# Kernel optimization log

Hardware: AMD Instinct MI355X
Metric: run time of the kernel (lower is better)

The kernel has to match this reference:

```python
import jax, jax.numpy as jnp
import numpy as np

NHLOG2PI = -0.5 * np.log(2.0 * np.pi)


def _log_bessel_i(nu, x):
    # log I_nu(x) via the uniform asymptotic expansion (A&S 9.7.7), accurate for large nu.
    # Replaces the original mpmath besseli loop with a device-friendly closed form.
    z = x / nu
    sq = jnp.sqrt(1.0 + z * z)
    eta = sq + jnp.log(z) - jnp.log1p(sq)
    t = 1.0 / sq
    u1 = (3.0 * t - 5.0 * t ** 3) / 24.0  # first correction term
    return nu * eta - 0.5 * jnp.log(2.0 * jnp.pi * nu) - 0.25 * jnp.log1p(z * z) + jnp.log1p(u1 / nu)


def _log_vmf_partition(d, kappa):
    # log C_d(kappa) = d*(-0.5 log 2pi) + s*log(kappa) - log I_s(kappa), s = d/2 - 1
    s = 0.5 * d - 1.0
    return d * NHLOG2PI + s * jnp.log(kappa) - _log_bessel_i(s, kappa)


def reference(id_samples, kappa_weight, prototypes, targets, project_dim):
    eps_n = 1e-12  # torch F.normalize eps
    eps_c = 1e-8   # torch cosine_similarity eps
    # --- sequential normalized EMA scatter-update of prototypes (faithful to per-sample loop) ---
    norm_samples = id_samples / jnp.maximum(
        jnp.linalg.norm(id_samples, axis=-1, keepdims=True), eps_n)

    def step(protos, inp):
        s_n, t = inp
        new = 0.05 * s_n + 0.95 * protos[t]
        new = new / jnp.maximum(jnp.linalg.norm(new), eps_n)
        return protos.at[t].set(new), None

    protos, _ = jax.lax.scan(step, prototypes, (norm_samples, targets))
    protos = jax.lax.stop_gradient(protos)  # original uses .data.detach()

    # --- cosine similarity [N, C] without materializing the repeated tensors ---
    x_n = id_samples / jnp.maximum(jnp.linalg.norm(id_samples, axis=-1, keepdims=True), eps_c)
    p_n = protos / jnp.maximum(jnp.linalg.norm(protos, axis=-1, keepdims=True), eps_c)
    cos = x_n @ p_n.T  # [N, C]

    kap = jax.nn.relu(kappa_weight)  # [C]
    logits = cos * kap[None, :]
    weight_before_exp = jnp.exp(_log_vmf_partition(float(project_dim), kap))[None, :]  # [1, C]

    # --- weighted vMF NLL ---
    num = weight_before_exp * jnp.exp(logits)
    pred = num / num.sum(-1, keepdims=True)
    p_t = jnp.take_along_axis(pred, targets[:, None], axis=1)[:, 0]
    return -jnp.mean(jnp.log(p_t + 1e-6))


def setup_inputs() -> dict:
    key = jax.random.key(0)
    k1, k2, k3 = jax.random.split(key, 3)
    N, C, D = 16384, 2048, 32
    return {
        "id_samples": jax.random.normal(k1, (N, D), dtype=jnp.float32),
        "kappa_weight": jax.random.uniform(k2, (C,), dtype=jnp.float32),
        "prototypes": jnp.zeros((C, D), dtype=jnp.float32),
        "targets": jax.random.randint(k3, (N,), 0, C),
        "project_dim": D,
    }
```

## Files before the change

### kernel.cpp

```cpp
#include <hip/hip_runtime.h>
#include <hip/hip_bf16.h>
#include <math.h>

#define D 32
#define CAP 64
#define PRE 24
#define PBW 8
#define SBT 512
#define SSM 16

typedef __attribute__((ext_vector_type(8))) short short8v;
typedef __attribute__((ext_vector_type(4))) float float4v;

static __device__ __forceinline__ unsigned short f2bf(float f) {
    union { __hip_bfloat16 h; unsigned short u; } cv;
    cv.h = __float2bfloat16(f);
    return cv.u;
}

__global__ void __launch_bounds__(64 * PBW)
k_pb(const float* __restrict__ x, const int* __restrict__ tgt,
     const float* __restrict__ p_in, const float* __restrict__ kw,
     unsigned short* __restrict__ qb, float* __restrict__ w,
     int N, int C, float dval) {
    __shared__ int lcnt[PBW];
    __shared__ int llist[PBW][CAP];
    int tid = threadIdx.x, b = blockIdx.x;
    int lane = tid & 63, wv = tid >> 6;
    int c0 = b * PBW;

    if (tid < PBW) lcnt[tid] = 0;
    __syncthreads();
    for (int i = tid; i < N; i += 64 * PBW) {
        int t = tgt[i];
        int r = t - c0;
        if ((unsigned)r < (unsigned)PBW) {
            int pos = atomicAdd(&lcnt[r], 1);
            if (pos < CAP) llist[r][pos] = i;
        }
    }
    __syncthreads();

    int c = c0 + wv;
    int e = lane & 31;
    float p = p_in[(size_t)c * D + e];
    int count = lcnt[wv];

    if (count <= PRE) {
        int idx = (lane < count) ? llist[wv][lane] : 0x7fffffff;
        int rank = 0;
        for (int j = 0; j < count; ++j) {
            int v = __shfl(idx, j);
            rank += (v < idx) ? 1 : 0;
        }
        int sorted = 0;
        for (int j = 0; j < count; ++j) {
            int v = __shfl(idx, j); int r = __shfl(rank, j);
            if (r == lane) sorted = v;
        }
        float vals[PRE];
#pragma unroll
        for (int it = 0; it < PRE; ++it)
            if (it < count) {
                int si = __shfl(sorted, it);
                vals[it] = x[(size_t)si * D + e];
            }
#pragma unroll
        for (int it = 0; it < PRE; ++it)
            if (it < count) {
                float v = vals[it];
                float ss = v * v;
                ss += __shfl_xor(ss, 16); ss += __shfl_xor(ss, 8); ss += __shfl_xor(ss, 4);
                ss += __shfl_xor(ss, 2);  ss += __shfl_xor(ss, 1);
                vals[it] = v / fmaxf(sqrtf(ss), 1e-12f);
            }
#pragma unroll
        for (int it = 0; it < PRE; ++it)
            if (it < count) {
                p = fmaf(0.05f, vals[it], 0.95f * p);
                float pp = p * p;
                pp += __shfl_xor(pp, 16); pp += __shfl_xor(pp, 8); pp += __shfl_xor(pp, 4);
                pp += __shfl_xor(pp, 2);  pp += __shfl_xor(pp, 1);
                p = p / fmaxf(sqrtf(pp), 1e-12f);
            }
    } else if (count <= CAP) {
        int idx = (lane < count) ? llist[wv][lane] : 0x7fffffff;
        for (int it = 0; it < count; ++it) {
            int mn = idx;
            mn = min(mn, __shfl_xor(mn, 32)); mn = min(mn, __shfl_xor(mn, 16));
            mn = min(mn, __shfl_xor(mn, 8));  mn = min(mn, __shfl_xor(mn, 4));
            mn = min(mn, __shfl_xor(mn, 2));  mn = min(mn, __shfl_xor(mn, 1));
            float v = x[(size_t)mn * D + e];
            float ss = v * v;
            ss += __shfl_xor(ss, 16); ss += __shfl_xor(ss, 8); ss += __shfl_xor(ss, 4);
            ss += __shfl_xor(ss, 2);  ss += __shfl_xor(ss, 1);
            float s = v / fmaxf(sqrtf(ss), 1e-12f);
            p = fmaf(0.05f, s, 0.95f * p);
            float pp = p * p;
            pp += __shfl_xor(pp, 16); pp += __shfl_xor(pp, 8); pp += __shfl_xor(pp, 4);
            pp += __shfl_xor(pp, 2);  pp += __shfl_xor(pp, 1);
            p = p / fmaxf(sqrtf(pp), 1e-12f);
            if (idx == mn) idx = 0x7fffffff;
        }
    } else {
        for (int ii = 0; ii < N; ii += 64) {
            unsigned long long m = __ballot(tgt[ii + lane] == c);
            while (m) {
                int j = __ffsll(m) - 1;
                m &= (m - 1);
                float v = x[(size_t)(ii + j) * D + e];
                float ss = v * v;
                ss += __shfl_xor(ss, 16); ss += __shfl_xor(ss, 8); ss += __shfl_xor(ss, 4);
                ss += __shfl_xor(ss, 2);  ss += __shfl_xor(ss, 1);
                float s = v / fmaxf(sqrtf(ss), 1e-12f);
                p = fmaf(0.05f, s, 0.95f * p);
                float pp = p * p;
                pp += __shfl_xor(pp, 16); pp += __shfl_xor(pp, 8); pp += __shfl_xor(pp, 4);
                pp += __shfl_xor(pp, 2);  pp += __shfl_xor(pp, 1);
                p = p / fmaxf(sqrtf(pp), 1e-12f);
            }
        }
    }

    float pp = p * p;
    pp += __shfl_xor(pp, 16); pp += __shfl_xor(pp, 8); pp += __shfl_xor(pp, 4);
    pp += __shfl_xor(pp, 2);  pp += __shfl_xor(pp, 1);
    float pn = p / fmaxf(sqrtf(pp), 1e-8f);
    float kap = fmaxf(kw[c], 0.0f);
    if (lane < D) qb[(size_t)c * D + e] = f2bf(kap * pn);
    if (lane == 0) {
        float nu = 0.5f * dval - 1.0f;
        float z  = kap / nu, z2 = z * z;
        float sq = sqrtf(1.0f + z2);
        float t  = 1.0f / sq;
        float u1 = (3.0f * t - 5.0f * t * t * t) * (1.0f / 24.0f);
        float lw = dval * (-0.918938533204672742f)
                 + nu * (logf(nu) + log1pf(sq) - sq)
                 + 0.5f * logf(6.2831853071795864f * nu)
                 + 0.25f * log1pf(z2)
                 - log1pf(u1 / nu);
        w[c] = __expf(lw);
    }
}

__global__ void __launch_bounds__(SBT)
k_score(const float* __restrict__ x, const int* __restrict__ tgt,
        const unsigned short* __restrict__ qb, const float* __restrict__ w,
        float* __restrict__ part, int N, int C) {
    __shared__ float Sl[8][SSM];
    __shared__ float Lt[SSM];
    int tid = threadIdx.x, b = blockIdx.x;
    int lane = tid & 63, wv = tid >> 6;
    int m = lane & 15, kg = lane >> 4, k0 = kg * 8;
    int s0 = b * SSM;

    short8v a0;
    {
        const float4* px = (const float4*)(x + (size_t)(s0 + m) * D + k0);
        float4 u0 = px[0], u1 = px[1];
        float ss = u0.x*u0.x + u0.y*u0.y + u0.z*u0.z + u0.w*u0.w
                 + u1.x*u1.x + u1.y*u1.y + u1.z*u1.z + u1.w*u1.w;
        ss += __shfl_xor(ss, 16); ss += __shfl_xor(ss, 32);
        float inv = 1.0f / fmaxf(sqrtf(ss), 1e-8f);
        a0[0] = (short)f2bf(u0.x*inv); a0[1] = (short)f2bf(u0.y*inv);
        a0[2] = (short)f2bf(u0.z*inv); a0[3] = (short)f2bf(u0.w*inv);
        a0[4] = (short)f2bf(u1.x*inv); a0[5] = (short)f2bf(u1.y*inv);
        a0[6] = (short)f2bf(u1.z*inv); a0[7] = (short)f2bf(u1.w*inv);
    }

    int tr0[4];
#pragma unroll
    for (int r = 0; r < 4; ++r) tr0[r] = tgt[s0 + kg * 4 + r];

    float4v z = {0.f, 0.f, 0.f, 0.f};
    float4v sa0 = z;
    int ntiles = C >> 7;
    for (int jt = 0; jt < ntiles; ++jt) {
        int c0 = (wv * ntiles + jt) * 16;
        short8v bfrag = *(const short8v*)(qb + (size_t)(c0 + m) * D + k0);
        float wl = w[c0 + m];
        float4v acc0 = __builtin_amdgcn_mfma_f32_16x16x32_bf16(a0, bfrag, z, 0, 0, 0);
#pragma unroll
        for (int r = 0; r < 4; ++r) {
            if (c0 + m == tr0[r]) Lt[kg * 4 + r] = acc0[r];
            sa0[r] = fmaf(wl, __expf(acc0[r]), sa0[r]);
        }
    }
#pragma unroll
    for (int off = 1; off < 16; off <<= 1) {
#pragma unroll
        for (int r = 0; r < 4; ++r) sa0[r] += __shfl_xor(sa0[r], off);
    }
    if (m == 0) {
#pragma unroll
        for (int r = 0; r < 4; ++r) Sl[wv][kg * 4 + r] = sa0[r];
    }
    __syncthreads();

    if (wv == 0) {
        float val = 0.f;
        if (lane < SSM) {
            int s = lane;
            float S = ((Sl[0][s] + Sl[1][s]) + (Sl[2][s] + Sl[3][s]))
                    + ((Sl[4][s] + Sl[5][s]) + (Sl[6][s] + Sl[7][s]));
            int t = tgt[s0 + s];
            val = logf(w[t] * __expf(Lt[s]) / S + 1e-6f);
        }
        val += __shfl_xor(val, 32); val += __shfl_xor(val, 16); val += __shfl_xor(val, 8);
        val += __shfl_xor(val, 4);  val += __shfl_xor(val, 2);  val += __shfl_xor(val, 1);
        if (lane == 0) part[b] = val;
    }
}

__global__ void k_out(const float* __restrict__ part, float* __restrict__ out,
                      int N, int nblk) {
    __shared__ float red[8];
    int tid = threadIdx.x, lane = tid & 63, wv = tid >> 6;
    float v = 0.f;
    if (tid < nblk)       v += part[tid];
    if (tid + 512 < nblk) v += part[tid + 512];
    v += __shfl_xor(v, 32); v += __shfl_xor(v, 16); v += __shfl_xor(v, 8);
    v += __shfl_xor(v, 4);  v += __shfl_xor(v, 2);  v += __shfl_xor(v, 1);
    if (lane == 0) red[wv] = v;
    __syncthreads();
    if (tid == 0)
        out[0] = -(((red[0] + red[1]) + (red[2] + red[3]))
                 + ((red[4] + red[5]) + (red[6] + red[7]))) / (float)N;
}

extern "C" void kernel_launch(void* const* d_in, const int* in_sizes, int n_in,
                              void* d_out, int out_size, void* d_ws, size_t ws_size,
                              hipStream_t stream) {
    const float* x    = (const float*)d_in[0];
    const float* kw   = (const float*)d_in[1];
    const float* p_in = (const float*)d_in[2];
    const int*   tgt  = (const int*)d_in[3];
    int C = in_sizes[1];
    int N = in_sizes[3];
    float dval = (float)(in_sizes[2] / C);
    int nblk = N / SSM;

    unsigned short* qb = (unsigned short*)d_ws;
    float* w    = (float*)(qb + (size_t)C * D);
    float* part = w + C;
    (void)n_in; (void)out_size; (void)ws_size;

    k_pb<<<C / PBW, 64 * PBW, 0, stream>>>(x, tgt, p_in, kw, qb, w, N, C, dval);
    k_score<<<nblk, SBT, 0, stream>>>(x, tgt, qb, w, part, N, C);
    k_out<<<1, 512, 0, stream>>>(part, (float*)d_out, N, nblk);
}
```

Before: 41.37 us.

## Map one thread per prototype class in EMA kernel with vectorized row loads

Restructures the prototype EMA kernel so each thread owns one class and keeps its 32-dim prototype in registers, instead of one 64-lane wavefront per class. Sample rows are read as float4 vectors, and per-class sample indices are ordered by a selection scan over shared memory. This removes the cross-lane shuffle reductions, the idle half-wave and most of the repeated full-target scanning, since far fewer blocks each scan the target list. In exchange the grid shrinks to a handful of blocks and each thread runs a serial chain of dependent-latency loads. A class with more than 33 samples falls back to a very slow serial scan over all targets.

Result: slower. 57.64 us (+39.3%).

```diff
diff --git a/kernel.cpp b/kernel.cpp
--- a/kernel.cpp
+++ b/kernel.cpp
@@ -3,9 +3,8 @@
 #include <math.h>
 
 #define D 32
-#define CAP 64
-#define PRE 24
-#define PBW 8
+#define CAP 33
+#define PBT 256
 #define SBT 512
 #define SSM 16
 
@@ -18,117 +17,105 @@
     return cv.u;
 }
 
-__global__ void __launch_bounds__(64 * PBW)
+static __device__ __forceinline__ void ema_step(float p[D], const float* __restrict__ x, int idx) {
+    float r0[D];
+#pragma unroll
+    for (int j = 0; j < D / 4; ++j) {
+        float4 v = ((const float4*)(x + (size_t)idx * D))[j];
+        r0[4*j] = v.x; r0[4*j+1] = v.y; r0[4*j+2] = v.z; r0[4*j+3] = v.w;
+    }
+    float s0 = 0.f, s1 = 0.f, s2 = 0.f, s3 = 0.f;
+#pragma unroll
+    for (int j = 0; j < D / 4; ++j) {
+        s0 = fmaf(r0[4*j],   r0[4*j],   s0);
+        s1 = fmaf(r0[4*j+1], r0[4*j+1], s1);
+        s2 = fmaf(r0[4*j+2], r0[4*j+2], s2);
+        s3 = fmaf(r0[4*j+3], r0[4*j+3], s3);
+    }
+    float inv = 1.0f / fmaxf(sqrtf((s0 + s1) + (s2 + s3)), 1e-12f);
+    float c05 = 0.05f * inv;
+#pragma unroll
+    for (int j = 0; j < D; ++j) p[j] = fmaf(c05, r0[j], 0.95f * p[j]);
+    float q0 = 0.f, q1 = 0.f, q2 = 0.f, q3 = 0.f;
+#pragma unroll
+    for (int j = 0; j < D / 4; ++j) {
+        q0 = fmaf(p[4*j],   p[4*j],   q0);
+        q1 = fmaf(p[4*j+1], p[4*j+1], q1);
+        q2 = fmaf(p[4*j+2], p[4*j+2], q2);
+        q3 = fmaf(p[4*j+3], p[4*j+3], q3);
+    }
+    float inv2 = 1.0f / fmaxf(sqrtf((q0 + q1) + (q2 + q3)), 1e-12f);
+#pragma unroll
+    for (int j = 0; j < D; ++j) p[j] *= inv2;
+}
+
+__global__ void __launch_bounds__(PBT)
 k_pb(const float* __restrict__ x, const int* __restrict__ tgt,
      const float* __restrict__ p_in, const float* __restrict__ kw,
      unsigned short* __restrict__ qb, float* __restrict__ w,
      int N, int C, float dval) {
-    __shared__ int lcnt[PBW];
-    __shared__ int llist[PBW][CAP];
+    __shared__ int lcnt[PBT];
+    __shared__ int llist[PBT][CAP];
     int tid = threadIdx.x, b = blockIdx.x;
-    int lane = tid & 63, wv = tid >> 6;
-    int c0 = b * PBW;
-
-    if (tid < PBW) lcnt[tid] = 0;
-    __syncthreads();
-    for (int i = tid; i < N; i += 64 * PBW) {
+    int c0 = b * PBT;
+    int c = c0 + tid;
+
+    lcnt[tid] = 0;
+    __syncthreads();
+#pragma unroll 4
+    for (int i = tid; i < N; i += PBT) {
         int t = tgt[i];
         int r = t - c0;
-        if ((unsigned)r < (unsigned)PBW) {
+        if ((unsigned)r < (unsigned)PBT) {
             int pos = atomicAdd(&lcnt[r], 1);
             if (pos < CAP) llist[r][pos] = i;
         }
     }
     __syncthreads();
 
-    int c = c0 + wv;
-    int e = lane & 31;
-    float p = p_in[(size_t)c * D + e];
-    int count = lcnt[wv];
-
-    if (count <= PRE) {
-        int idx = (lane < count) ? llist[wv][lane] : 0x7fffffff;
-        int rank = 0;
-        for (int j = 0; j < count; ++j) {
-            int v = __shfl(idx, j);
-            rank += (v < idx) ? 1 : 0;
-        }
-        int sorted = 0;
-        for (int j = 0; j < count; ++j) {
-            int v = __shfl(idx, j); int r = __shfl(rank, j);
-            if (r == lane) sorted = v;
-        }
-        float vals[PRE];
-#pragma unroll
-        for (int it = 0; it < PRE; ++it)
-            if (it < count) {
-                int si = __shfl(sorted, it);
-                vals[it] = x[(size_t)si * D + e];
+    int cnt = lcnt[tid];
+
+    float p[D];
+#pragma unroll
+    for (int j = 0; j < D / 4; ++j) {
+        float4 v = ((const float4*)(p_in + (size_t)c * D))[j];
+        p[4*j] = v.x; p[4*j+1] = v.y; p[4*j+2] = v.z; p[4*j+3] = v.w;
+    }
+
+    if (cnt <= CAP) {
+        int last = -1;
+        for (int step = 0; step < cnt; ++step) {
+            int best = 0x7fffffff;
+            for (int k = 0; k < cnt; ++k) {
+                int v = llist[tid][k];
+                if (v > last && v < best) best = v;
             }
-#pragma unroll
-        for (int it = 0; it < PRE; ++it)
-            if (it < count) {
-                float v = vals[it];
-                float ss = v * v;
-                ss += __shfl_xor(ss, 16); ss += __shfl_xor(ss, 8); ss += __shfl_xor(ss, 4);
-                ss += __shfl_xor(ss, 2);  ss += __shfl_xor(ss, 1);
-                vals[it] = v / fmaxf(sqrtf(ss), 1e-12f);
-            }
-#pragma unroll
-        for (int it = 0; it < PRE; ++it)
-            if (it < count) {
-                p = fmaf(0.05f, vals[it], 0.95f * p);
-                float pp = p * p;
-                pp += __shfl_xor(pp, 16); pp += __shfl_xor(pp, 8); pp += __shfl_xor(pp, 4);
-                pp += __shfl_xor(pp, 2);  pp += __shfl_xor(pp, 1);
-                p = p / fmaxf(sqrtf(pp), 1e-12f);
-            }
-    } else if (count <= CAP) {
-        int idx = (lane < count) ? llist[wv][lane] : 0x7fffffff;
-        for (int it = 0; it < count; ++it) {
-            int mn = idx;
-            mn = min(mn, __shfl_xor(mn, 32)); mn = min(mn, __shfl_xor(mn, 16));
-            mn = min(mn, __shfl_xor(mn, 8));  mn = min(mn, __shfl_xor(mn, 4));
-            mn = min(mn, __shfl_xor(mn, 2));  mn = min(mn, __shfl_xor(mn, 1));
-            float v = x[(size_t)mn * D + e];
-            float ss = v * v;
-            ss += __shfl_xor(ss, 16); ss += __shfl_xor(ss, 8); ss += __shfl_xor(ss, 4);
-            ss += __shfl_xor(ss, 2);  ss += __shfl_xor(ss, 1);
-            float s = v / fmaxf(sqrtf(ss), 1e-12f);
-            p = fmaf(0.05f, s, 0.95f * p);
-            float pp = p * p;
-            pp += __shfl_xor(pp, 16); pp += __shfl_xor(pp, 8); pp += __shfl_xor(pp, 4);
-            pp += __shfl_xor(pp, 2);  pp += __shfl_xor(pp, 1);
-            p = p / fmaxf(sqrtf(pp), 1e-12f);
-            if (idx == mn) idx = 0x7fffffff;
+            last = best;
+            ema_step(p, x, best);
         }
     } else {
-        for (int ii = 0; ii < N; ii += 64) {
-            unsigned long long m = __ballot(tgt[ii + lane] == c);
-            while (m) {
-                int j = __ffsll(m) - 1;
-                m &= (m - 1);
-                float v = x[(size_t)(ii + j) * D + e];
-                float ss = v * v;
-                ss += __shfl_xor(ss, 16); ss += __shfl_xor(ss, 8); ss += __shfl_xor(ss, 4);
-                ss += __shfl_xor(ss, 2);  ss += __shfl_xor(ss, 1);
-                float s = v / fmaxf(sqrtf(ss), 1e-12f);
-                p = fmaf(0.05f, s, 0.95f * p);
-                float pp = p * p;
-                pp += __shfl_xor(pp, 16); pp += __shfl_xor(pp, 8); pp += __shfl_xor(pp, 4);
-                pp += __shfl_xor(pp, 2);  pp += __shfl_xor(pp, 1);
-                p = p / fmaxf(sqrtf(pp), 1e-12f);
-            }
-        }
-    }
-
-    float pp = p * p;
-    pp += __shfl_xor(pp, 16); pp += __shfl_xor(pp, 8); pp += __shfl_xor(pp, 4);
-    pp += __shfl_xor(pp, 2);  pp += __shfl_xor(pp, 1);
-    float pn = p / fmaxf(sqrtf(pp), 1e-8f);
+        for (int i = 0; i < N; ++i)
+            if (tgt[i] == c) ema_step(p, x, i);
+    }
+
+    float q0 = 0.f, q1 = 0.f, q2 = 0.f, q3 = 0.f;
+#pragma unroll
+    for (int j = 0; j < D / 4; ++j) {
+        q0 = fmaf(p[4*j],   p[4*j],   q0);
+        q1 = fmaf(p[4*j+1], p[4*j+1], q1);
+        q2 = fmaf(p[4*j+2], p[4*j+2], q2);
+        q3 = fmaf(p[4*j+3], p[4*j+3], q3);
+    }
+    float pninv = 1.0f / fmaxf(sqrtf((q0 + q1) + (q2 + q3)), 1e-8f);
     float kap = fmaxf(kw[c], 0.0f);
-    if (lane < D) qb[(size_t)c * D + e] = f2bf(kap * pn);
-    if (lane == 0) {
+    float scale = kap * pninv;
+#pragma unroll
+    for (int j = 0; j < D / 2; ++j) {
+        unsigned int lo = f2bf(scale * p[2*j]);
+        unsigned int hi = f2bf(scale * p[2*j+1]);
+        ((unsigned int*)(qb + (size_t)c * D))[j] = lo | (hi << 16);
+    }
+    {
         float nu = 0.5f * dval - 1.0f;
         float z  = kap / nu, z2 = z * z;
         float sq = sqrtf(1.0f + z2);
@@ -245,7 +232,7 @@
     float* part = w + C;
     (void)n_in; (void)out_size; (void)ws_size;
 
-    k_pb<<<C / PBW, 64 * PBW, 0, stream>>>(x, tgt, p_in, kw, qb, w, N, C, dval);
+    k_pb<<<C / PBT, PBT, 0, stream>>>(x, tgt, p_in, kw, qb, w, N, C, dval);
     k_score<<<nblk, SBT, 0, stream>>>(x, tgt, qb, w, part, N, C);
     k_out<<<1, 512, 0, stream>>>(part, (float*)d_out, N, nblk);
 }
```

## Replace sequential prototype EMA with Gram-matrix coefficient recurrence per class

Applied to the files above, without the earlier changes.

Reformulates the per-class normalized EMA scan as a linear combination of normalized samples. Norms are tracked through a Gram matrix of sample dot products computed in shared memory, so the serial chain of cross-lane reductions is replaced by scalar coefficient updates and one final combination. It also halves classes per block to four and lowers the list cap to 28. The cost is extra shared memory, O(n^2) dot products, and a fully unrolled 28-coefficient register array, which may raise register pressure. Rounding can also differ from the step-by-step renormalization.

After: 42.81 us. 1.03x slower.

```diff
diff --git a/kernel.cpp b/kernel.cpp
--- a/kernel.cpp
+++ b/kernel.cpp
@@ -3,9 +3,8 @@
 #include <math.h>
 
 #define D 32
-#define CAP 64
-#define PRE 24
-#define PBW 8
+#define CAP 28
+#define CPB 4
 #define SBT 512
 #define SSM 16
 
@@ -18,101 +17,126 @@
     return cv.u;
 }
 
-__global__ void __launch_bounds__(64 * PBW)
-k_pb(const float* __restrict__ x, const int* __restrict__ tgt,
-     const float* __restrict__ p_in, const float* __restrict__ kw,
-     unsigned short* __restrict__ qb, float* __restrict__ w,
-     int N, int C, float dval) {
-    __shared__ int lcnt[PBW];
-    __shared__ int llist[PBW][CAP];
+__global__ void __launch_bounds__(64 * CPB)
+k_solve(const float* __restrict__ x, const int* __restrict__ tgt,
+        const float* __restrict__ p_in, const float* __restrict__ kw,
+        unsigned short* __restrict__ qb, float* __restrict__ w,
+        int N, int C, float dval) {
+    __shared__ int   lcnt[CPB];
+    __shared__ int   llist[CPB][CAP];
+    __shared__ float R[CPB][29][33];
+    __shared__ float G[CPB][28][28];
+    __shared__ float gP[CPB][29];
     int tid = threadIdx.x, b = blockIdx.x;
     int lane = tid & 63, wv = tid >> 6;
-    int c0 = b * PBW;
-
-    if (tid < PBW) lcnt[tid] = 0;
-    __syncthreads();
-    for (int i = tid; i < N; i += 64 * PBW) {
-        int t = tgt[i];
-        int r = t - c0;
-        if ((unsigned)r < (unsigned)PBW) {
+    int c = b * CPB + wv;
+    int e = lane & 31;
+
+    if (tid < CPB) lcnt[tid] = 0;
+    __syncthreads();
+    for (int i = tid; i < N; i += 64 * CPB) {
+        int r = tgt[i] - b * CPB;
+        if ((unsigned)r < (unsigned)CPB) {
             int pos = atomicAdd(&lcnt[r], 1);
             if (pos < CAP) llist[r][pos] = i;
         }
     }
     __syncthreads();
 
-    int c = c0 + wv;
-    int e = lane & 31;
-    float p = p_in[(size_t)c * D + e];
-    int count = lcnt[wv];
-
-    if (count <= PRE) {
-        int idx = (lane < count) ? llist[wv][lane] : 0x7fffffff;
+    int n = lcnt[wv];
+    float kap = fmaxf(kw[c], 0.0f);
+
+    if (n <= CAP) {
+        int idx = (lane < n) ? llist[wv][lane] : 0x7fffffff;
         int rank = 0;
-        for (int j = 0; j < count; ++j) {
-            int v = __shfl(idx, j);
-            rank += (v < idx) ? 1 : 0;
-        }
-        int sorted = 0;
-        for (int j = 0; j < count; ++j) {
+        for (int j = 0; j < n; ++j) { int v = __shfl(idx, j); rank += (v < idx) ? 1 : 0; }
+        int sorted = idx;
+        for (int j = 0; j < n; ++j) {
             int v = __shfl(idx, j); int r = __shfl(rank, j);
             if (r == lane) sorted = v;
         }
-        float vals[PRE];
-#pragma unroll
-        for (int it = 0; it < PRE; ++it)
-            if (it < count) {
-                int si = __shfl(sorted, it);
-                vals[it] = x[(size_t)si * D + e];
-            }
-#pragma unroll
-        for (int it = 0; it < PRE; ++it)
-            if (it < count) {
-                float v = vals[it];
-                float ss = v * v;
-                ss += __shfl_xor(ss, 16); ss += __shfl_xor(ss, 8); ss += __shfl_xor(ss, 4);
-                ss += __shfl_xor(ss, 2);  ss += __shfl_xor(ss, 1);
-                vals[it] = v / fmaxf(sqrtf(ss), 1e-12f);
-            }
-#pragma unroll
-        for (int it = 0; it < PRE; ++it)
-            if (it < count) {
-                p = fmaf(0.05f, vals[it], 0.95f * p);
-                float pp = p * p;
-                pp += __shfl_xor(pp, 16); pp += __shfl_xor(pp, 8); pp += __shfl_xor(pp, 4);
-                pp += __shfl_xor(pp, 2);  pp += __shfl_xor(pp, 1);
-                p = p / fmaxf(sqrtf(pp), 1e-12f);
-            }
-    } else if (count <= CAP) {
-        int idx = (lane < count) ? llist[wv][lane] : 0x7fffffff;
-        for (int it = 0; it < count; ++it) {
-            int mn = idx;
-            mn = min(mn, __shfl_xor(mn, 32)); mn = min(mn, __shfl_xor(mn, 16));
-            mn = min(mn, __shfl_xor(mn, 8));  mn = min(mn, __shfl_xor(mn, 4));
-            mn = min(mn, __shfl_xor(mn, 2));  mn = min(mn, __shfl_xor(mn, 1));
-            float v = x[(size_t)mn * D + e];
+        if (lane < D) R[wv][28][e] = p_in[(size_t)c * D + e];
+        int half = lane >> 5;
+        for (int r0 = 0; r0 < n; r0 += 2) {
+            int r = r0 + half;
+            int ok = (r < n);
+            int si = __shfl(sorted, ok ? r : 0);
+            float v = ok ? x[(size_t)si * D + e] : 0.f;
             float ss = v * v;
             ss += __shfl_xor(ss, 16); ss += __shfl_xor(ss, 8); ss += __shfl_xor(ss, 4);
             ss += __shfl_xor(ss, 2);  ss += __shfl_xor(ss, 1);
-            float s = v / fmaxf(sqrtf(ss), 1e-12f);
-            p = fmaf(0.05f, s, 0.95f * p);
-            float pp = p * p;
-            pp += __shfl_xor(pp, 16); pp += __shfl_xor(pp, 8); pp += __shfl_xor(pp, 4);
-            pp += __shfl_xor(pp, 2);  pp += __shfl_xor(pp, 1);
-            p = p / fmaxf(sqrtf(pp), 1e-12f);
-            if (idx == mn) idx = 0x7fffffff;
-        }
+            if (ok) R[wv][r][e] = v / fmaxf(sqrtf(ss), 1e-12f);
+        }
+
+        int T = n * (n - 1) / 2;
+        for (int q = lane; q < T; q += 64) {
+            int k = (int)((1.0f + sqrtf(1.0f + 8.0f * (float)q)) * 0.5f);
+            while (k * (k - 1) / 2 > q) --k;
+            while ((k + 1) * k / 2 <= q) ++k;
+            int j = q - k * (k - 1) / 2;
+            float a0 = 0.f, a1 = 0.f, a2 = 0.f, a3 = 0.f;
+            for (int d4 = 0; d4 < D; d4 += 4) {
+                a0 = fmaf(R[wv][k][d4],     R[wv][j][d4],     a0);
+                a1 = fmaf(R[wv][k][d4 + 1], R[wv][j][d4 + 1], a1);
+                a2 = fmaf(R[wv][k][d4 + 2], R[wv][j][d4 + 2], a2);
+                a3 = fmaf(R[wv][k][d4 + 3], R[wv][j][d4 + 3], a3);
+            }
+            G[wv][k][j] = (a0 + a1) + (a2 + a3);
+        }
+        for (int k = lane; k <= n; k += 64) {
+            int kk = (k < n) ? k : 28;
+            float a0 = 0.f, a1 = 0.f, a2 = 0.f, a3 = 0.f;
+            for (int d4 = 0; d4 < D; d4 += 4) {
+                a0 = fmaf(R[wv][kk][d4],     R[wv][28][d4],     a0);
+                a1 = fmaf(R[wv][kk][d4 + 1], R[wv][28][d4 + 1], a1);
+                a2 = fmaf(R[wv][kk][d4 + 2], R[wv][28][d4 + 2], a2);
+                a3 = fmaf(R[wv][kk][d4 + 3], R[wv][28][d4 + 3], a3);
+            }
+            gP[wv][(k < n) ? k : 28] = (a0 + a1) + (a2 + a3);
+        }
+
+        float cc[CAP];
+        float cp = 1.0f, U2 = gP[wv][28];
+#pragma unroll
+        for (int kk = 0; kk < CAP; ++kk) {
+            if (kk < n) {
+                float dsum = cp * gP[wv][kk];
+#pragma unroll
+                for (int j = 0; j < CAP; ++j)
+                    if (j < kk) dsum = fmaf(cc[j], G[wv][kk][j], dsum);
+                float m2 = 0.0025f + fmaf(0.9025f, U2, 0.095f * dsum);
+                float m = fmaxf(sqrtf(m2), 1e-12f);
+                float binv = 0.95f / m;
+                cp *= binv;
+#pragma unroll
+                for (int j = 0; j < CAP; ++j)
+                    if (j < kk) cc[j] *= binv;
+                cc[kk] = 0.05f / m;
+                U2 = 1.0f;
+            }
+        }
+
+        float u = cp * R[wv][28][e];
+#pragma unroll
+        for (int j = 0; j < CAP; ++j)
+            if (j < n) u = fmaf(cc[j], R[wv][j][e], u);
+        float ss = u * u;
+        ss += __shfl_xor(ss, 16); ss += __shfl_xor(ss, 8); ss += __shfl_xor(ss, 4);
+        ss += __shfl_xor(ss, 2);  ss += __shfl_xor(ss, 1);
+        float pninv = 1.0f / fmaxf(sqrtf(ss), 1e-8f);
+        if (lane < D) qb[(size_t)c * D + e] = f2bf(kap * pninv * u);
     } else {
+        float p = p_in[(size_t)c * D + e];
         for (int ii = 0; ii < N; ii += 64) {
-            unsigned long long m = __ballot(tgt[ii + lane] == c);
-            while (m) {
-                int j = __ffsll(m) - 1;
-                m &= (m - 1);
+            unsigned long long mb = __ballot(tgt[ii + lane] == c);
+            while (mb) {
+                int j = __ffsll(mb) - 1;
+                mb &= (mb - 1);
                 float v = x[(size_t)(ii + j) * D + e];
-                float ss = v * v;
-                ss += __shfl_xor(ss, 16); ss += __shfl_xor(ss, 8); ss += __shfl_xor(ss, 4);
-                ss += __shfl_xor(ss, 2);  ss += __shfl_xor(ss, 1);
-                float s = v / fmaxf(sqrtf(ss), 1e-12f);
+                float s2 = v * v;
+                s2 += __shfl_xor(s2, 16); s2 += __shfl_xor(s2, 8); s2 += __shfl_xor(s2, 4);
+                s2 += __shfl_xor(s2, 2);  s2 += __shfl_xor(s2, 1);
+                float s = v / fmaxf(sqrtf(s2), 1e-12f);
                 p = fmaf(0.05f, s, 0.95f * p);
                 float pp = p * p;
                 pp += __shfl_xor(pp, 16); pp += __shfl_xor(pp, 8); pp += __shfl_xor(pp, 4);
@@ -120,14 +144,13 @@
                 p = p / fmaxf(sqrtf(pp), 1e-12f);
             }
         }
-    }
-
-    float pp = p * p;
-    pp += __shfl_xor(pp, 16); pp += __shfl_xor(pp, 8); pp += __shfl_xor(pp, 4);
-    pp += __shfl_xor(pp, 2);  pp += __shfl_xor(pp, 1);
-    float pn = p / fmaxf(sqrtf(pp), 1e-8f);
-    float kap = fmaxf(kw[c], 0.0f);
-    if (lane < D) qb[(size_t)c * D + e] = f2bf(kap * pn);
+        float pp = p * p;
+        pp += __shfl_xor(pp, 16); pp += __shfl_xor(pp, 8); pp += __shfl_xor(pp, 4);
+        pp += __shfl_xor(pp, 2);  pp += __shfl_xor(pp, 1);
+        float pn = p / fmaxf(sqrtf(pp), 1e-8f);
+        if (lane < D) qb[(size_t)c * D + e] = f2bf(kap * pn);
+    }
+
     if (lane == 0) {
         float nu = 0.5f * dval - 1.0f;
         float z  = kap / nu, z2 = z * z;
@@ -245,7 +268,7 @@
     float* part = w + C;
     (void)n_in; (void)out_size; (void)ws_size;
 
-    k_pb<<<C / PBW, 64 * PBW, 0, stream>>>(x, tgt, p_in, kw, qb, w, N, C, dval);
+    k_solve<<<C / CPB, 64 * CPB, 0, stream>>>(x, tgt, p_in, kw, qb, w, N, C, dval);
     k_score<<<nblk, SBT, 0, stream>>>(x, tgt, qb, w, part, N, C);
     k_out<<<1, 512, 0, stream>>>(part, (float*)d_out, N, nblk);
 }
```
